# Kernel tuning notes

Hardware: AMD Instinct MI355X
Metric: run time of the kernel (lower is better)

Reference implementation:

```python
import jax, jax.numpy as jnp
import numpy as np

H, ND, RD, VD = 16, 128, 64, 128  # heads, nope/rope/v head dims
EPS = 1e-6


def rmsnorm(x, g):
    return x * jax.lax.rsqrt(jnp.mean(x * x, axis=-1, keepdims=True) + EPS) * g


def apply_rope(x, cos, sin):
    # x: [B,T,h,D]; cos/sin: [1,T,1,D/2]; interleaved pair rotation
    x1, x2 = x[..., 0::2], x[..., 1::2]
    o1 = x1 * cos - x2 * sin
    o2 = x1 * sin + x2 * cos
    return jnp.stack([o1, o2], axis=-1).reshape(x.shape)


def setup_inputs() -> dict:
    key = jax.random.key(0)
    ks = jax.random.split(key, 10)
    B, T, D = 2, 2048, 2048
    QR, KVR = 1536, 512
    s = 0.02
    return {
        "x": jax.random.normal(ks[0], (B, T, D), jnp.float32),
        "w_cq": jax.random.normal(ks[1], (D, QR), jnp.float32) * s,
        "g_q": jnp.ones((QR,), jnp.float32),
        "w_ckv": jax.random.normal(ks[2], (D, KVR), jnp.float32) * s,
        "g_kv": jnp.ones((KVR,), jnp.float32),
        "w_dq_nope": jax.random.normal(ks[3], (QR, H * ND), jnp.float32) * s,
        "w_dq_rope": jax.random.normal(ks[4], (QR, H * RD), jnp.float32) * s,
        "w_dk_nope": jax.random.normal(ks[5], (KVR, H * ND), jnp.float32) * s,
        "w_dv": jax.random.normal(ks[6], (KVR, H * VD), jnp.float32) * s,
        "w_k_rope": jax.random.normal(ks[7], (D, RD), jnp.float32) * s,
        "w_out": jax.random.normal(ks[8], (H * VD, D), jnp.float32) * s,
    }


def reference(x, w_cq, g_q, w_ckv, g_kv, w_dq_nope, w_dq_rope,
              w_dk_nope, w_dv, w_k_rope, w_out):
    B, T, D = x.shape
    # low-rank latents + RMSNorm
    q_lat = rmsnorm(x @ w_cq, g_q)          # [B,T,QR]
    kv_lat = rmsnorm(x @ w_ckv, g_kv)        # [B,T,KVR]
    q_nope = (q_lat @ w_dq_nope).reshape(B, T, H, ND)
    q_rope = (q_lat @ w_dq_rope).reshape(B, T, H, RD)
    k_nope = (kv_lat @ w_dk_nope).reshape(B, T, H, ND)
    v = (kv_lat @ w_dv).reshape(B, T, H, VD)
    k_rope = (x @ w_k_rope).reshape(B, T, 1, RD)  # shared across heads
    # RoPE (start_pos = 0, no past_kv)
    pos = jnp.arange(T, dtype=jnp.float32)
    inv_freq = 1.0 / (10000.0 ** (jnp.arange(0, RD, 2, dtype=jnp.float32) / RD))
    ang = pos[:, None] * inv_freq[None, :]               # [T, RD/2]
    cos = jnp.cos(ang)[None, :, None, :]
    sin = jnp.sin(ang)[None, :, None, :]
    q_rope = apply_rope(q_rope, cos, sin)
    k_rope = apply_rope(k_rope, cos, sin)
    k_rope = jnp.broadcast_to(k_rope, (B, T, H, RD))
    q = jnp.concatenate([q_nope, q_rope], axis=-1).transpose(0, 2, 1, 3)  # [B,H,T,ND+RD]
    k = jnp.concatenate([k_nope, k_rope], axis=-1).transpose(0, 2, 1, 3)
    v_t = v.transpose(0, 2, 1, 3)                                        # [B,H,T,VD]
    # causal SDPA, scale = 1/sqrt(head_dim)
    scale = 1.0 / jnp.sqrt(jnp.asarray(ND + RD, jnp.float32))
    scores = jnp.einsum('bhqd,bhkd->bhqk', q, k) * scale
    causal = jnp.tril(jnp.ones((T, T), dtype=bool))
    scores = jnp.where(causal[None, None], scores, -jnp.inf)
    attn = jax.nn.softmax(scores, axis=-1)
    out = jnp.einsum('bhqk,bhkd->bhqd', attn, v_t)
    out = out.transpose(0, 2, 1, 3).reshape(B, T, H * VD) @ w_out        # [B,T,D]
    return out, k, v_t
```

## Files before the change

### kernel.cpp

```cpp
#include <hip/hip_runtime.h>
#include <cstdint>
#include <cstddef>

typedef _Float16 HT;
typedef _Float16 h8 __attribute__((ext_vector_type(8)));
typedef _Float16 h4 __attribute__((ext_vector_type(4)));
typedef float f32x4 __attribute__((ext_vector_type(4)));

constexpr int Tn  = 2048;
constexpr int Dm  = 2048;
constexpr int Hh  = 16;
constexpr int RDc = 64;
constexpr int QRc = 1536;
constexpr int KVRc= 512;
constexpr int BT  = 4096;

#define VWAIT(N) asm volatile("s_waitcnt vmcnt(" #N ")" ::: "memory")
#define SBAR()   __builtin_amdgcn_s_barrier()

__device__ __forceinline__ f32x4 mfma16(h8 a, h8 b, f32x4 c) {
    return __builtin_amdgcn_mfma_f32_16x16x32_f16(a, b, c, 0, 0, 0);
}
__device__ __forceinline__ void gload_lds16(const void* g, void* l) {
    __builtin_amdgcn_global_load_lds(
        (const __attribute__((address_space(1))) unsigned int*)g,
        (__attribute__((address_space(3))) unsigned int*)l, 16, 0, 0);
}

__global__ __launch_bounds__(256)
void cstab_kernel(float2* __restrict__ cs)
{
    const int idx = blockIdx.x * 256 + threadIdx.x;
    const int t = idx >> 5, i = idx & 31;
    const float ang = (float)t * exp2f(-(float)i * (13.287712379549449f / 32.f));
    cs[idx] = make_float2(cosf(ang), sinf(ang));
}

__global__ __launch_bounds__(256)
void wtrans_kernel(const float* __restrict__ src, HT* __restrict__ dst,
                   int K, int N)
{
    __shared__ float Ts[64][65];
    const int k0 = blockIdx.y * 64, n0 = blockIdx.x * 64;
    const int tid = threadIdx.x;
    {
        const int r = tid >> 2, c0 = (tid & 3) * 16;
        const float* s = src + (size_t)(k0 + r) * N + n0 + c0;
        #pragma unroll
        for (int j = 0; j < 4; j++)
            *reinterpret_cast<f32x4*>(&Ts[r][c0 + j * 4]) = *reinterpret_cast<const f32x4*>(s + j * 4);
    }
    __syncthreads();
    {
        const int c = tid >> 2, kq = (tid & 3) * 16;
        h8 o0, o1;
        #pragma unroll
        for (int j = 0; j < 8; j++) { o0[j] = (HT)Ts[kq + j][c]; o1[j] = (HT)Ts[kq + 8 + j][c]; }
        HT* d = dst + (size_t)(n0 + c) * K + k0 + kq;
        *reinterpret_cast<h8*>(d)     = o0;
        *reinterpret_cast<h8*>(d + 8) = o1;
    }
}

__global__ __launch_bounds__(256)
void convx_kernel(const float* __restrict__ x, HT* __restrict__ x16)
{
    const size_t i = ((size_t)blockIdx.x * 256 + threadIdx.x) * 8;
    f32x4 a = *reinterpret_cast<const f32x4*>(x + i);
    f32x4 b = *reinterpret_cast<const f32x4*>(x + i + 4);
    h8 v;
    #pragma unroll
    for (int j = 0; j < 4; j++) { v[j] = (HT)a[j]; v[4 + j] = (HT)b[j]; }
    *reinterpret_cast<h8*>(x16 + i) = v;
}

template<int EPI>
__global__ __launch_bounds__(256)
void gemm16d(const HT* __restrict__ A, const HT* __restrict__ Bt, const int K,
             HT* __restrict__ o1, HT* __restrict__ o2, HT* __restrict__ o3,
             float* __restrict__ f1, float* __restrict__ f2,
             const float2* __restrict__ cstab)
{
    __shared__ HT As[2][4096];
    __shared__ HT Bs[2][4096];

    const int tid  = threadIdx.x;
    const int lane = tid & 63;
    const int l15  = lane & 15, l4 = lane >> 4;
    const int w    = tid >> 6;
    const int wr   = w >> 1, wc = w & 1;
    const int m0   = blockIdx.y * 128;
    const int n0   = blockIdx.x * 128;

    f32x4 acc[4][4] = {};
    const int nk = K >> 5;

#define GSTAGE(as_, bs_, kt_) do {                                             \
    _Pragma("unroll")                                                          \
    for (int i_ = 0; i_ < 2; i_++) {                                           \
        const int row_ = (w * 2 + i_) * 16 + (lane >> 2);                      \
        gload_lds16(A  + (size_t)(m0 + row_) * K + (kt_) + (lane & 3) * 8,     \
                    (as_) + (w * 2 + i_) * 512);                               \
        gload_lds16(Bt + (size_t)(n0 + row_) * K + (kt_) + (lane & 3) * 8,     \
                    (bs_) + (w * 2 + i_) * 512);                               \
    } } while (0)

    GSTAGE(As[0], Bs[0], 0);

    for (int kt = 0; kt < nk; kt++) {
        HT* as = As[kt & 1];
        HT* bs = Bs[kt & 1];
        if (kt + 1 < nk) {
            GSTAGE(As[(kt + 1) & 1], Bs[(kt + 1) & 1], (kt + 1) * 32);
            VWAIT(4);
        } else {
            VWAIT(0);
        }
        SBAR();

        h8 af[4], bf[4];
        #pragma unroll
        for (int f = 0; f < 4; f++)
            af[f] = *reinterpret_cast<const h8*>(&as[(wr * 64 + f * 16 + l15) * 32 + l4 * 8]);
        #pragma unroll
        for (int g = 0; g < 4; g++)
            bf[g] = *reinterpret_cast<const h8*>(&bs[(wc * 64 + g * 16 + l15) * 32 + l4 * 8]);
        #pragma unroll
        for (int f = 0; f < 4; f++)
            #pragma unroll
            for (int g = 0; g < 4; g++)
                acc[f][g] = mfma16(af[f], bf[g], acc[f][g]);
        SBAR();
    }
#undef GSTAGE

    #pragma unroll
    for (int f = 0; f < 4; f++) {
        #pragma unroll
        for (int g = 0; g < 4; g++) {
            const int row = m0 + wr * 64 + f * 16 + l4 * 4;
            const int col = n0 + wc * 64 + g * 16 + l15;
            if constexpr (EPI == 3) {
                #pragma unroll
                for (int r = 0; r < 4; r++)
                    f1[(size_t)(row + r) * 2048 + col] = acc[f][g][r];
            } else if constexpr (EPI == 0) {
                if (col < 1536) {
                    #pragma unroll
                    for (int r = 0; r < 4; r++)
                        o1[(size_t)(row + r) * 1536 + col] = (HT)acc[f][g][r];
                } else if (col < 2048) {
                    #pragma unroll
                    for (int r = 0; r < 4; r++)
                        o2[(size_t)(row + r) * 512 + (col - 1536)] = (HT)acc[f][g][r];
                } else if (col < 2112) {
                    const int cc = col - 2048;
                    const int i = cc >> 1;
                    const bool odd = cc & 1;
                    #pragma unroll
                    for (int r = 0; r < 4; r++) {
                        const int t = (row + r) & (Tn - 1);
                        const float2 cs = cstab[t * 32 + i];
                        const float v = acc[f][g][r];
                        const float p = __shfl_xor(v, 1);
                        const float ov = odd ? p * cs.y + v * cs.x : v * cs.x - p * cs.y;
                        o3[(size_t)(row + r) * 64 + cc] = (HT)ov;
                    }
                }
            } else if constexpr (EPI == 1) {
                if (col < 2048) {
                    #pragma unroll
                    for (int r = 0; r < 4; r++)
                        o1[(size_t)(row + r) * 2048 + col] = (HT)acc[f][g][r];
                } else {
                    const int cc = col - 2048;
                    const int i = (cc & 63) >> 1;
                    const bool odd = cc & 1;
                    #pragma unroll
                    for (int r = 0; r < 4; r++) {
                        const int t = (row + r) & (Tn - 1);
                        const float2 cs = cstab[t * 32 + i];
                        const float v = acc[f][g][r];
                        const float p = __shfl_xor(v, 1);
                        const float ov = odd ? p * cs.y + v * cs.x : v * cs.x - p * cs.y;
                        o2[(size_t)(row + r) * 1024 + cc] = (HT)ov;
                    }
                }
            } else {
                if (col < 2048) {
                    const int h = col >> 7, d = col & 127;
                    #pragma unroll
                    for (int r = 0; r < 4; r++) {
                        const int rw = row + r;
                        const int b = rw >> 11, t = rw & (Tn - 1);
                        o1[(size_t)rw * 2048 + col] = (HT)acc[f][g][r];
                        f1[((size_t)(b * Hh + h) * Tn + t) * 192 + d] = acc[f][g][r];
                    }
                } else {
                    const int c2 = col - 2048;
                    const int h = c2 >> 7, d = c2 & 127;
                    const int b = row >> 11, t0 = row & (Tn - 1);
                    h4 pk;
                    #pragma unroll
                    for (int r = 0; r < 4; r++) {
                        f2[((size_t)(b * Hh + h) * Tn + t0 + r) * 128 + d] = acc[f][g][r];
                        pk[r] = (HT)acc[f][g][r];
                    }
                    *reinterpret_cast<h4*>(&o3[((size_t)(b * Hh + h) * 128 + d) * Tn + t0]) = pk;
                }
            }
        }
    }
}

__global__ __launch_bounds__(256)
void kropebc_kernel(const HT* __restrict__ kr16, float* __restrict__ out_k)
{
    const int idx = blockIdx.x * 256 + threadIdx.x;
    const int j4 = (idx & 15) * 4;
    const int t  = (idx >> 4) & (Tn - 1);
    const int b  = idx >> 15;
    h4 v = *reinterpret_cast<const h4*>(&kr16[((size_t)(b * Tn + t)) * 64 + j4]);
    f32x4 f;
    #pragma unroll
    for (int r = 0; r < 4; r++) f[r] = (float)v[r];
    #pragma unroll
    for (int h = 0; h < Hh; h++)
        *reinterpret_cast<f32x4*>(&out_k[((size_t)(b * Hh + h) * Tn + t) * 192 + 128 + j4]) = f;
}

__global__ __launch_bounds__(256)
void rmsnorm_kernel(HT* __restrict__ X, const float* __restrict__ g, int N)
{
    const int row = blockIdx.x;
    HT* x = X + (size_t)row * N;
    float ss = 0.f;
    for (int i = threadIdx.x * 8; i < N; i += 2048) {
        h8 v = *reinterpret_cast<const h8*>(&x[i]);
        #pragma unroll
        for (int j = 0; j < 8; j++) { float f = (float)v[j]; ss += f * f; }
    }
    #pragma unroll
    for (int sh = 32; sh >= 1; sh >>= 1) ss += __shfl_xor(ss, sh);
    __shared__ float red[4];
    if ((threadIdx.x & 63) == 0) red[threadIdx.x >> 6] = ss;
    __syncthreads();
    const float tot = red[0] + red[1] + red[2] + red[3];
    const float scale = rsqrtf(tot / (float)N + 1e-6f);
    for (int i = threadIdx.x * 8; i < N; i += 2048) {
        h8 v = *reinterpret_cast<const h8*>(&x[i]);
        f32x4 g0 = *reinterpret_cast<const f32x4*>(&g[i]);
        f32x4 g1 = *reinterpret_cast<const f32x4*>(&g[i + 4]);
        #pragma unroll
        for (int j = 0; j < 4; j++) { v[j]   = (HT)((float)v[j]   * scale * g0[j]);
                                      v[4+j] = (HT)((float)v[4+j] * scale * g1[j]); }
        *reinterpret_cast<h8*>(&x[i]) = v;
    }
}

__global__ __launch_bounds__(512, 4)
void attn5_kernel(const HT* __restrict__ qn, const HT* __restrict__ qr,
                  const HT* __restrict__ kn, const HT* __restrict__ kr16,
                  const HT* __restrict__ vt, HT* __restrict__ ao)
{
    __shared__ HT Ks_n[64 * 128];
    __shared__ HT Ks_r[64 * 64];
    __shared__ HT Vs[128 * 64];
    __shared__ HT Ps[8][16][72];

    const int tid  = threadIdx.x;
    const int lane = tid & 63;
    const int l15  = lane & 15, l4 = lane >> 4;
    const int w    = tid >> 6;

    const int bid  = blockIdx.x;
    const int tile = 15 - (bid >> 5);
    const int h    = bid & 15;
    const int b    = (bid >> 4) & 1;

    const size_t bT = (size_t)b * Tn;
    const HT* vt_h = vt + ((size_t)(b * Hh + h) * 128) * Tn;

    const int qw = tile * 128 + 16 * w;

    h8 aq[6];
    {
        const size_t rq = bT + qw + l15;
        const HT* pn = qn + rq * 2048 + h * 128 + l4 * 8;
        #pragma unroll
        for (int f = 0; f < 4; f++) aq[f] = *reinterpret_cast<const h8*>(pn + f * 32);
        const HT* pr = qr + rq * 1024 + h * 64 + l4 * 8;
        aq[4] = *reinterpret_cast<const h8*>(pr);
        aq[5] = *reinterpret_cast<const h8*>(pr + 32);
    }

    f32x4 o[8] = {};
    float m_i[4] = {-1e30f, -1e30f, -1e30f, -1e30f};
    float l_i[4] = {0.f, 0.f, 0.f, 0.f};

    const int nkb = (tile + 1) * 2;
    for (int kb64 = 0; kb64 < nkb; kb64++) {
        const int kb = kb64 * 64;
        __syncthreads();
        #pragma unroll
        for (int i = 0; i < 2; i++) {
            const int cc = w * 2 + i;
            const int r  = cc * 4 + l4;
            const int cl = (l15 & 8) | ((l15 & 7) ^ (r & 7));
            gload_lds16(kn + (bT + kb + r) * 2048 + h * 128 + cl * 8,
                        &Ks_n[cc * 512]);
        }
        {
            const int r  = w * 8 + (lane >> 3);
            const int cl = (lane & 7) ^ (r & 7);
            gload_lds16(kr16 + (bT + kb + r) * 64 + cl * 8,
                        &Ks_r[w * 512]);
        }
        #pragma unroll
        for (int i = 0; i < 2; i++) {
            const int cc = w * 2 + i;
            const int d  = cc * 8 + (lane >> 3);
            const int cl = (lane & 7) ^ (d & 7);
            gload_lds16(vt_h + (size_t)d * Tn + kb + cl * 8,
                        &Vs[cc * 512]);
        }
        __syncthreads();

        if (kb <= qw + 15) {
            f32x4 s[4] = {};
            #pragma unroll
            for (int c = 0; c < 4; c++) {
                const int kr = c * 16 + l15;
                const int sw = (kr & 7) << 4;
                const char* kbase = (const char*)Ks_n + kr * 256;
                #pragma unroll
                for (int f = 0; f < 4; f++)
                    s[c] = mfma16(aq[f], *(const h8*)(kbase + ((f * 64 + l4 * 16) ^ sw)), s[c]);
                const char* rbase = (const char*)Ks_r + kr * 128;
                s[c] = mfma16(aq[4], *(const h8*)(rbase + ((l4 * 16) ^ sw)), s[c]);
                s[c] = mfma16(aq[5], *(const h8*)(rbase + ((64 + l4 * 16) ^ sw)), s[c]);
            }
            const float scl = 0.07216878364870323f;
            float al[4];
            #pragma unroll
            for (int r = 0; r < 4; r++) {
                const int qrow = qw + l4 * 4 + r;
                float a[4];
                #pragma unroll
                for (int c = 0; c < 4; c++)
                    a[c] = (kb + c * 16 + l15 <= qrow) ? s[c][r] * scl : -1e30f;
                float mx = fmaxf(fmaxf(a[0], a[1]), fmaxf(a[2], a[3]));
                #pragma unroll
                for (int sh = 1; sh < 16; sh <<= 1) mx = fmaxf(mx, __shfl_xor(mx, sh));
                const float mn = fmaxf(m_i[r], mx);
                const float alpha = __expf(m_i[r] - mn);
                m_i[r] = mn;
                float rs = 0.f;
                #pragma unroll
                for (int c = 0; c < 4; c++) {
                    const float e = __expf(a[c] - mn);
                    rs += e;
                    Ps[w][l4 * 4 + r][c * 16 + l15] = (HT)e;
                }
                #pragma unroll
                for (int sh = 1; sh < 16; sh <<= 1) rs += __shfl_xor(rs, sh);
                l_i[r] = l_i[r] * alpha + rs;
                al[r] = alpha;
            }
            #pragma unroll
            for (int g = 0; g < 8; g++)
                #pragma unroll
                for (int r = 0; r < 4; r++) o[g][r] *= al[r];

            const h8 ap0 = *reinterpret_cast<const h8*>(&Ps[w][l15][l4 * 8]);
            const h8 ap1 = *reinterpret_cast<const h8*>(&Ps[w][l15][32 + l4 * 8]);

            #pragma unroll
            for (int g = 0; g < 8; g++) {
                const int d = g * 16 + l15;
                const int sw = (d & 7) << 4;
                const char* vbase = (const char*)Vs + d * 128;
                h8 v0 = *(const h8*)(vbase + ((l4 * 16) ^ sw));
                h8 v1 = *(const h8*)(vbase + ((64 + l4 * 16) ^ sw));
                o[g] = mfma16(ap0, v0, o[g]);
                o[g] = mfma16(ap1, v1, o[g]);
            }
        }
    }

    const size_t orow = bT + qw + l4 * 4;
    #pragma unroll
    for (int r = 0; r < 4; r++) {
        const float inv = 1.0f / l_i[r];
        HT* dst = ao + (orow + r) * 2048 + h * 128 + l15;
        #pragma unroll
        for (int g = 0; g < 8; g++) dst[g * 16] = (HT)(o[g][r] * inv);
    }
}

extern "C" void kernel_launch(void* const* d_in, const int* in_sizes, int n_in,
                              void* d_out, int out_size, void* d_ws, size_t ws_size,
                              hipStream_t stream)
{
    const float* x     = (const float*)d_in[0];
    const float* w_cq  = (const float*)d_in[1];
    const float* g_q   = (const float*)d_in[2];
    const float* w_ckv = (const float*)d_in[3];
    const float* g_kv  = (const float*)d_in[4];
    const float* w_dqn = (const float*)d_in[5];
    const float* w_dqr = (const float*)d_in[6];
    const float* w_dkn = (const float*)d_in[7];
    const float* w_dv  = (const float*)d_in[8];
    const float* w_kr  = (const float*)d_in[9];
    const float* w_out = (const float*)d_in[10];

    char* ws = (char*)d_ws;
    HT* cqT   = (HT*)(ws + 0);
    HT* ckvT  = (HT*)(ws + 6291456);
    HT* krT   = (HT*)(ws + 8388608);
    HT* dqnT  = (HT*)(ws + 8912896);
    HT* dqrT  = (HT*)(ws + 15204352);
    HT* dknT  = (HT*)(ws + 18350080);
    HT* dvT   = (HT*)(ws + 20447232);
    HT* outT  = (HT*)(ws + 22544384);
    HT* cq    = (HT*)(ws + 30932992);
    HT* ckv   = (HT*)(ws + 43515904);
    HT* qn    = (HT*)(ws + 47710208);
    HT* qr    = (HT*)(ws + 64487424);
    HT* kn    = (HT*)(ws + 72876032);
    HT* kr16  = (HT*)(ws + 89653248);
    HT* vt    = (HT*)(ws + 0);
    HT* x16   = qn;
    HT* ao    = qn;

    float* out_o = (float*)d_out;
    float* out_k = out_o + (size_t)BT * Dm;
    float* out_v = out_k + (size_t)2 * Hh * Tn * 192;
    float2* cstab = (float2*)out_v;

    const dim3 blk(256);

    cstab_kernel<<<dim3(256), blk, 0, stream>>>(cstab);
    wtrans_kernel<<<dim3(QRc/64,  Dm/64), blk, 0, stream>>>(w_cq,  cqT,  Dm,  QRc);
    wtrans_kernel<<<dim3(KVRc/64, Dm/64), blk, 0, stream>>>(w_ckv, ckvT, Dm,  KVRc);
    wtrans_kernel<<<dim3(RDc/64,  Dm/64), blk, 0, stream>>>(w_kr,  krT,  Dm,  RDc);
    wtrans_kernel<<<dim3(Dm/64, QRc/64),  blk, 0, stream>>>(w_dqn, dqnT, QRc, Dm);
    wtrans_kernel<<<dim3((Hh*RDc)/64, QRc/64), blk, 0, stream>>>(w_dqr, dqrT, QRc, Hh*RDc);
    wtrans_kernel<<<dim3(Dm/64, KVRc/64), blk, 0, stream>>>(w_dkn, dknT, KVRc, Dm);
    wtrans_kernel<<<dim3(Dm/64, KVRc/64), blk, 0, stream>>>(w_dv,  dvT,  KVRc, Dm);
    wtrans_kernel<<<dim3(Dm/64, Dm/64),   blk, 0, stream>>>(w_out, outT, Dm,  Dm);

    convx_kernel<<<dim3(4096), blk, 0, stream>>>(x, x16);

    gemm16d<0><<<dim3(17, BT/128), blk, 0, stream>>>(x16, cqT, Dm,
        cq, ckv, kr16, nullptr, nullptr, cstab);
    kropebc_kernel<<<dim3(256), blk, 0, stream>>>(kr16, out_k);

    rmsnorm_kernel<<<dim3(BT), blk, 0, stream>>>(cq,  g_q,  QRc);
    rmsnorm_kernel<<<dim3(BT), blk, 0, stream>>>(ckv, g_kv, KVRc);

    gemm16d<1><<<dim3(24, BT/128), blk, 0, stream>>>(cq, dqnT, QRc,
        qn, qr, nullptr, nullptr, nullptr, cstab);
    gemm16d<2><<<dim3(32, BT/128), blk, 0, stream>>>(ckv, dknT, KVRc,
        kn, nullptr, vt, out_k, out_v, nullptr);

    attn5_kernel<<<dim3(512), dim3(512), 0, stream>>>(qn, qr, kn, kr16, vt, ao);

    gemm16d<3><<<dim3(16, BT/128), blk, 0, stream>>>(ao, outT, Dm,
        nullptr, nullptr, nullptr, out_o, nullptr, nullptr);
}
```

Before: 385.1 us.

## Halve attention query tile to 64 rows, load rope keys directly, add setprio

The attention kernel now uses 256-thread blocks covering 64 query rows instead of 512 threads covering 128, launching twice as many blocks. This gives finer causal load balance and skips less masked work per block. The shared rope-key tile is dropped: each wave reads the rope key fragments straight from global memory (L2-cached) inside the score loop. s_setprio wrappers are added around the MFMA sections. The trade-off is less K/V reuse per block, since each key tile is staged into LDS by twice as many blocks, plus global-load latency inside the MFMA loop.

```diff
diff --git a/kernel.cpp b/kernel.cpp
--- a/kernel.cpp
+++ b/kernel.cpp
@@ -258,15 +258,14 @@
     }
 }
 
-__global__ __launch_bounds__(512, 4)
-void attn5_kernel(const HT* __restrict__ qn, const HT* __restrict__ qr,
+__global__ __launch_bounds__(256)
+void attn6_kernel(const HT* __restrict__ qn, const HT* __restrict__ qr,
                   const HT* __restrict__ kn, const HT* __restrict__ kr16,
                   const HT* __restrict__ vt, HT* __restrict__ ao)
 {
     __shared__ HT Ks_n[64 * 128];
-    __shared__ HT Ks_r[64 * 64];
     __shared__ HT Vs[128 * 64];
-    __shared__ HT Ps[8][16][72];
+    __shared__ HT Ps[4][16][72];
 
     const int tid  = threadIdx.x;
     const int lane = tid & 63;
@@ -274,14 +273,15 @@
     const int w    = tid >> 6;
 
     const int bid  = blockIdx.x;
-    const int tile = 15 - (bid >> 5);
+    const int tile = 31 - (bid >> 5);
     const int h    = bid & 15;
     const int b    = (bid >> 4) & 1;
 
     const size_t bT = (size_t)b * Tn;
     const HT* vt_h = vt + ((size_t)(b * Hh + h) * 128) * Tn;
-
-    const int qw = tile * 128 + 16 * w;
+    const HT* krb  = kr16 + bT * 64;
+
+    const int qw = tile * 64 + 16 * w;
 
     h8 aq[6];
     {
@@ -298,48 +298,44 @@
     float m_i[4] = {-1e30f, -1e30f, -1e30f, -1e30f};
     float l_i[4] = {0.f, 0.f, 0.f, 0.f};
 
-    const int nkb = (tile + 1) * 2;
+    const int nkb = tile + 1;
     for (int kb64 = 0; kb64 < nkb; kb64++) {
         const int kb = kb64 * 64;
         __syncthreads();
         #pragma unroll
-        for (int i = 0; i < 2; i++) {
-            const int cc = w * 2 + i;
-            const int r  = cc * 4 + l4;
+        for (int j = 0; j < 4; j++) {
+            const int r = (w * 4 + j) * 4 + l4;
             const int cl = (l15 & 8) | ((l15 & 7) ^ (r & 7));
             gload_lds16(kn + (bT + kb + r) * 2048 + h * 128 + cl * 8,
-                        &Ks_n[cc * 512]);
+                        &Ks_n[(w * 4 + j) * 512]);
         }
-        {
-            const int r  = w * 8 + (lane >> 3);
-            const int cl = (lane & 7) ^ (r & 7);
-            gload_lds16(kr16 + (bT + kb + r) * 64 + cl * 8,
-                        &Ks_r[w * 512]);
-        }
-        #pragma unroll
-        for (int i = 0; i < 2; i++) {
-            const int cc = w * 2 + i;
-            const int d  = cc * 8 + (lane >> 3);
+        #pragma unroll
+        for (int j = 0; j < 4; j++) {
+            const int d = (w * 4 + j) * 8 + (lane >> 3);
             const int cl = (lane & 7) ^ (d & 7);
             gload_lds16(vt_h + (size_t)d * Tn + kb + cl * 8,
-                        &Vs[cc * 512]);
+                        &Vs[(w * 4 + j) * 512]);
         }
         __syncthreads();
 
         if (kb <= qw + 15) {
             f32x4 s[4] = {};
+            __builtin_amdgcn_s_setprio(1);
             #pragma unroll
             for (int c = 0; c < 4; c++) {
                 const int kr = c * 16 + l15;
+                const HT* rp = krb + (size_t)(kb + kr) * 64 + l4 * 8;
+                const h8 br0 = *reinterpret_cast<const h8*>(rp);
+                const h8 br1 = *reinterpret_cast<const h8*>(rp + 32);
                 const int sw = (kr & 7) << 4;
                 const char* kbase = (const char*)Ks_n + kr * 256;
                 #pragma unroll
                 for (int f = 0; f < 4; f++)
                     s[c] = mfma16(aq[f], *(const h8*)(kbase + ((f * 64 + l4 * 16) ^ sw)), s[c]);
-                const char* rbase = (const char*)Ks_r + kr * 128;
-                s[c] = mfma16(aq[4], *(const h8*)(rbase + ((l4 * 16) ^ sw)), s[c]);
-                s[c] = mfma16(aq[5], *(const h8*)(rbase + ((64 + l4 * 16) ^ sw)), s[c]);
+                s[c] = mfma16(aq[4], br0, s[c]);
+                s[c] = mfma16(aq[5], br1, s[c]);
             }
+            __builtin_amdgcn_s_setprio(0);
             const float scl = 0.07216878364870323f;
             float al[4];
             #pragma unroll
@@ -375,6 +371,7 @@
             const h8 ap0 = *reinterpret_cast<const h8*>(&Ps[w][l15][l4 * 8]);
             const h8 ap1 = *reinterpret_cast<const h8*>(&Ps[w][l15][32 + l4 * 8]);
 
+            __builtin_amdgcn_s_setprio(1);
             #pragma unroll
             for (int g = 0; g < 8; g++) {
                 const int d = g * 16 + l15;
@@ -385,6 +382,7 @@
                 o[g] = mfma16(ap0, v0, o[g]);
                 o[g] = mfma16(ap1, v1, o[g]);
             }
+            __builtin_amdgcn_s_setprio(0);
         }
     }
 
@@ -464,7 +462,7 @@
     gemm16d<2><<<dim3(32, BT/128), blk, 0, stream>>>(ckv, dknT, KVRc,
         kn, nullptr, vt, out_k, out_v, nullptr);
 
-    attn5_kernel<<<dim3(512), dim3(512), 0, stream>>>(qn, qr, kn, kr16, vt, ao);
+    attn6_kernel<<<dim3(1024), blk, 0, stream>>>(qn, qr, kn, kr16, vt, ao);
 
     gemm16d<3><<<dim3(16, BT/128), blk, 0, stream>>>(ao, outT, Dm,
         nullptr, nullptr, nullptr, out_o, nullptr, nullptr);
```

New measurement: 382.7 us. About the same (-0.6%).
